# Kernel optimization log

Measured on AMD Instinct MI355X. Metric: run time of the kernel, lower is better.

Reference implementation:

```python
import jax, jax.numpy as jnp
import numpy as np

HIDDEN = 256
B, SQ, SKV = 8, 2048, 2048
SCALE = float(np.sqrt(HIDDEN / 2.0))  # module uses sqrt(hidden_dim/2)


def setup_inputs() -> dict:
    key = jax.random.key(0)
    ks = jax.random.split(key, 9)
    s = 1.0 / np.sqrt(HIDDEN)
    return {
        "query": jax.random.normal(ks[0], (B, SQ, HIDDEN), jnp.float32),
        "key": jax.random.normal(ks[1], (B, SKV, HIDDEN), jnp.float32),
        "value": jax.random.normal(ks[2], (B, SKV, HIDDEN), jnp.float32),
        "Wq": jax.random.uniform(ks[3], (HIDDEN, HIDDEN), jnp.float32, -s, s),
        "bq": jax.random.uniform(ks[4], (HIDDEN,), jnp.float32, -s, s),
        "Wk": jax.random.uniform(ks[5], (HIDDEN, HIDDEN), jnp.float32, -s, s),
        "bk": jax.random.uniform(ks[6], (HIDDEN,), jnp.float32, -s, s),
        "Wv": jax.random.uniform(ks[7], (HIDDEN, HIDDEN), jnp.float32, -s, s),
        "bv": jax.random.uniform(ks[8], (HIDDEN,), jnp.float32, -s, s),
    }


def reference(query, key, value, Wq, bq, Wk, bk, Wv, bv):
    # Linear projections (torch Linear: x @ W.T + b)
    Q = jnp.einsum('bsd,ed->bse', query, Wq) + bq  # [B,SQ,H]
    K = jnp.einsum('bsd,ed->bse', key, Wk) + bk    # [B,SKV,H]
    V = jnp.einsum('bsd,ed->bse', value, Wv) + bv  # [B,SKV,H]
    scores = jnp.einsum('bqd,bkd->bqk', Q, K) / SCALE  # [B,SQ,SKV]
    weights = jax.nn.softmax(scores, axis=-1)
    return jnp.einsum('bqk,bkd->bqd', weights, V)  # [B,SQ,H]
```

## Files before the change

kernel.cpp:

```cpp
#include <hip/hip_runtime.h>

#define HID 256
#define NB 8
#define SQL 2048
#define SKV 2048
#define SPLIT 4
#define KPB (SKV / SPLIT)
#define KVB 32
#define NT (KPB / KVB)
#define NROW (NB * SQL)

typedef __attribute__((ext_vector_type(8))) short bf16x8;
typedef __attribute__((ext_vector_type(4))) float f32x4;

static __device__ __forceinline__ unsigned short f2bf(float x) {
  union { float f; unsigned int u; } v; v.f = x;
  unsigned int r = v.u + 0x7FFFu + ((v.u >> 16) & 1u);
  return (unsigned short)(r >> 16);
}

__global__ void wconv_kernel(const float* __restrict__ Wq, const float* __restrict__ Wk,
                             const float* __restrict__ Wv, unsigned short* __restrict__ out) {
  int i = blockIdx.x * blockDim.x + threadIdx.x;
  if (i >= 3 * HID * HID) return;
  const float* src = (i < HID * HID) ? Wq : (i < 2 * HID * HID ? Wk : Wv);
  out[i] = f2bf(src[i & (HID * HID - 1)]);
}

__global__ __launch_bounds__(512, 4) void proj_kernel(
    const float* __restrict__ query, const float* __restrict__ key, const float* __restrict__ value,
    const unsigned short* __restrict__ Wb,
    const float* __restrict__ bq, const float* __restrict__ bk, const float* __restrict__ bv,
    unsigned short* __restrict__ Qb, unsigned short* __restrict__ Kb, unsigned short* __restrict__ Vtb) {
  __shared__ __align__(16) char wl[65536];
  int tid = threadIdx.x;
  int wave = tid >> 6, lane = tid & 63, lr = lane & 15, lg = lane >> 4;
  int blk = blockIdx.x;
  int mat = blk >> 8;
  int rem = blk & 255;
  int b = rem >> 5;
  int rt = (rem >> 1) & 15;
  int et = rem & 1;

  const float* X = (mat == 0) ? query : (mat == 1 ? key : value);
  const float* bias = (mat == 0) ? bq : (mat == 1 ? bk : bv);
  const char* Wsrc = (const char*)(Wb + mat * HID * HID + et * 128 * HID);

#pragma unroll
  for (int i = 0; i < 8; i++) {
    int c = i * 512 + tid;
    int e = c >> 5;
    int glo = e * 512 + (((c & 31) ^ (e & 7)) << 4);
    __builtin_amdgcn_global_load_lds(
        (const __attribute__((address_space(1))) unsigned int*)(Wsrc + glo),
        (__attribute__((address_space(3))) unsigned int*)(wl + c * 16), 16, 0, 0);
  }

  int row_a = rt * 128 + wave * 16 + lr;
  const float* xrow = X + ((size_t)(b * SQL + row_a)) * HID;
  bf16x8 af[8];
#pragma unroll
  for (int s = 0; s < 8; s++) {
    const float4* p = (const float4*)(xrow + s * 32 + lg * 8);
    float4 x0 = p[0], x1 = p[1];
    bf16x8 a;
    a[0] = (short)f2bf(x0.x); a[1] = (short)f2bf(x0.y); a[2] = (short)f2bf(x0.z); a[3] = (short)f2bf(x0.w);
    a[4] = (short)f2bf(x1.x); a[5] = (short)f2bf(x1.y); a[6] = (short)f2bf(x1.z); a[7] = (short)f2bf(x1.w);
    af[s] = a;
  }
  __syncthreads();

  int row_c = rt * 128 + wave * 16 + lg * 4;
#pragma unroll
  for (int eo = 0; eo < 8; eo++) {
    f32x4 acc = (f32x4){0.f, 0.f, 0.f, 0.f};
    int eL = eo * 16 + lr;
#pragma unroll
    for (int sl = 0; sl < 8; sl++) {
      bf16x8 bfr = *(const bf16x8*)(wl + eL * 512 + (((sl * 4 + lg) ^ (eL & 7)) << 4));
      acc = __builtin_amdgcn_mfma_f32_16x16x32_bf16(af[sl], bfr, acc, 0, 0, 0);
    }
    int e = et * 128 + eo * 16 + lr;
    float bv_ = bias[e];
    if (mat < 2) {
      unsigned short* dst = (mat == 0 ? Qb : Kb) + (size_t)(b * SQL) * HID;
#pragma unroll
      for (int i = 0; i < 4; i++)
        dst[(size_t)(row_c + i) * HID + e] = f2bf(acc[i] + bv_);
    } else {
      ushort4 v;
      v.x = f2bf(acc[0] + bv_); v.y = f2bf(acc[1] + bv_);
      v.z = f2bf(acc[2] + bv_); v.w = f2bf(acc[3] + bv_);
      *(ushort4*)(Vtb + ((size_t)(b * HID + e)) * SKV + row_c) = v;
    }
  }
}

__global__ __launch_bounds__(256, 2) void attn_kernel(
    const unsigned short* __restrict__ Qb, const unsigned short* __restrict__ Kb,
    const unsigned short* __restrict__ Vtb, unsigned short* __restrict__ Op,
    float* __restrict__ Ml) {
  extern __shared__ char smem[];
  int tid = threadIdx.x;
  int wave = tid >> 6, lane = tid & 63, l15 = lane & 15, g = lane >> 4;
  int L = (blockIdx.x & 7) * 64 + (blockIdx.x >> 3);
  int b = L >> 6, sp = (L >> 4) & 3, qt = L & 15;
  int q0 = qt * 128 + wave * 32;

  const char* Kc0 = (const char*)(Kb + ((size_t)b * SKV + (size_t)sp * KPB) * HID);
  const char* Vc0 = (const char*)(Vtb + (size_t)b * HID * SKV + (size_t)sp * KPB);

  int offK[4], offV[4];
#pragma unroll
  for (int i = 0; i < 4; i++) {
    int idx = i * 256 + tid;
    int r = idx >> 5, cs = idx & 31;
    int sig = 8 * ((r & 15) >> 2) + (r & 3) + 4 * (r >> 4);
    offK[i] = sig * 512 + ((cs ^ r) << 4);
    int rv = idx >> 3, pp = idx & 7;
    int p = pp ^ (rv & 7);
    int d = 2 * rv + (p >> 2), c = p & 3;
    offV[i] = d * (SKV * 2) + c * 16;
  }

  auto stage = [&](int t, char* kb, char* vb) {
    const char* Ks = Kc0 + t * (KVB * HID * 2);
    const char* Vs = Vc0 + t * (KVB * 2);
#pragma unroll
    for (int i = 0; i < 4; i++)
      __builtin_amdgcn_global_load_lds(
          (const __attribute__((address_space(1))) unsigned int*)(Ks + offK[i]),
          (__attribute__((address_space(3))) unsigned int*)(kb + (i * 256 + tid) * 16),
          16, 0, 0);
#pragma unroll
    for (int i = 0; i < 4; i++)
      __builtin_amdgcn_global_load_lds(
          (const __attribute__((address_space(1))) unsigned int*)(Vs + offV[i]),
          (__attribute__((address_space(3))) unsigned int*)(vb + (i * 256 + tid) * 16),
          16, 0, 0);
  };

  bf16x8 qfa[8], qfb[8];
  {
    const unsigned short* qa = Qb + ((size_t)(b * SQL + q0 + l15)) * HID + g * 8;
    const unsigned short* qb2 = qa + 16 * HID;
#pragma unroll
    for (int s = 0; s < 8; s++) {
      qfa[s] = *(const bf16x8*)(qa + s * 32);
      qfb[s] = *(const bf16x8*)(qb2 + s * 32);
    }
  }

  f32x4 acc0[16], acc1[16];
#pragma unroll
  for (int dt = 0; dt < 16; dt++) {
    acc0[dt] = (f32x4){0.f, 0.f, 0.f, 0.f};
    acc1[dt] = (f32x4){0.f, 0.f, 0.f, 0.f};
  }
  float m0 = -1e30f, l0 = 0.f, m1 = -1e30f, l1 = 0.f;
  const float kC = 1.44269504088896341f / 11.3137084989847604f;

  auto step = [&](const char* kb, const char* vb) {
    f32x4 p0a = (f32x4){0.f,0.f,0.f,0.f}, p1a = (f32x4){0.f,0.f,0.f,0.f};
    f32x4 p0b = (f32x4){0.f,0.f,0.f,0.f}, p1b = (f32x4){0.f,0.f,0.f,0.f};
#pragma unroll
    for (int s = 0; s < 8; s++) {
      int c0 = s * 4 + g;
      bf16x8 kf0 = *(const bf16x8*)(kb + l15 * 512 + ((c0 ^ l15) << 4));
      bf16x8 kf1 = *(const bf16x8*)(kb + (16 + l15) * 512 + (((c0 ^ l15) ^ 16) << 4));
      p0a = __builtin_amdgcn_mfma_f32_16x16x32_bf16(kf0, qfa[s], p0a, 0, 0, 0);
      p1a = __builtin_amdgcn_mfma_f32_16x16x32_bf16(kf1, qfa[s], p1a, 0, 0, 0);
      p0b = __builtin_amdgcn_mfma_f32_16x16x32_bf16(kf0, qfb[s], p0b, 0, 0, 0);
      p1b = __builtin_amdgcn_mfma_f32_16x16x32_bf16(kf1, qfb[s], p1b, 0, 0, 0);
    }

    float ta = fmaxf(fmaxf(fmaxf(p0a[0], p0a[1]), fmaxf(p0a[2], p0a[3])),
                     fmaxf(fmaxf(p1a[0], p1a[1]), fmaxf(p1a[2], p1a[3])));
    float tb = fmaxf(fmaxf(fmaxf(p0b[0], p0b[1]), fmaxf(p0b[2], p0b[3])),
                     fmaxf(fmaxf(p1b[0], p1b[1]), fmaxf(p1b[2], p1b[3])));
    ta = fmaxf(ta, __shfl_xor(ta, 16, 64)); tb = fmaxf(tb, __shfl_xor(tb, 16, 64));
    ta = fmaxf(ta, __shfl_xor(ta, 32, 64)); tb = fmaxf(tb, __shfl_xor(tb, 32, 64));
    float msa = ta * kC, msb = tb * kC;
    if (!__all(msa <= m0 + 8.0f)) {
      float mn = fmaxf(m0, msa);
      float al = exp2f(m0 - mn);
      l0 *= al; m0 = mn;
#pragma unroll
      for (int dt = 0; dt < 16; dt++)
#pragma unroll
        for (int i = 0; i < 4; i++) acc0[dt][i] *= al;
    }
    if (!__all(msb <= m1 + 8.0f)) {
      float mn = fmaxf(m1, msb);
      float al = exp2f(m1 - mn);
      l1 *= al; m1 = mn;
#pragma unroll
      for (int dt = 0; dt < 16; dt++)
#pragma unroll
        for (int i = 0; i < 4; i++) acc1[dt][i] *= al;
    }
#pragma unroll
    for (int i = 0; i < 4; i++) {
      p0a[i] = exp2f(fmaf(p0a[i], kC, -m0)); p1a[i] = exp2f(fmaf(p1a[i], kC, -m0));
      p0b[i] = exp2f(fmaf(p0b[i], kC, -m1)); p1b[i] = exp2f(fmaf(p1b[i], kC, -m1));
    }
    float sa = (p0a[0] + p0a[1]) + (p0a[2] + p0a[3]) + (p1a[0] + p1a[1]) + (p1a[2] + p1a[3]);
    float sb = (p0b[0] + p0b[1]) + (p0b[2] + p0b[3]) + (p1b[0] + p1b[1]) + (p1b[2] + p1b[3]);
    sa += __shfl_xor(sa, 16, 64); sb += __shfl_xor(sb, 16, 64);
    sa += __shfl_xor(sa, 32, 64); sb += __shfl_xor(sb, 32, 64);
    l0 += sa; l1 += sb;

    unsigned wa0, wa1, wa2, wa3, wb0, wb1, wb2, wb3;
    asm("v_cvt_pk_bf16_f32 %0, %1, %2" : "=v"(wa0) : "v"(p0a[0]), "v"(p0a[1]));
    asm("v_cvt_pk_bf16_f32 %0, %1, %2" : "=v"(wa1) : "v"(p0a[2]), "v"(p0a[3]));
    asm("v_cvt_pk_bf16_f32 %0, %1, %2" : "=v"(wa2) : "v"(p1a[0]), "v"(p1a[1]));
    asm("v_cvt_pk_bf16_f32 %0, %1, %2" : "=v"(wa3) : "v"(p1a[2]), "v"(p1a[3]));
    asm("v_cvt_pk_bf16_f32 %0, %1, %2" : "=v"(wb0) : "v"(p0b[0]), "v"(p0b[1]));
    asm("v_cvt_pk_bf16_f32 %0, %1, %2" : "=v"(wb1) : "v"(p0b[2]), "v"(p0b[3]));
    asm("v_cvt_pk_bf16_f32 %0, %1, %2" : "=v"(wb2) : "v"(p1b[0]), "v"(p1b[1]));
    asm("v_cvt_pk_bf16_f32 %0, %1, %2" : "=v"(wb3) : "v"(p1b[2]), "v"(p1b[3]));
    union { unsigned u[4]; bf16x8 v; } pa, pb;
    pa.u[0] = wa0; pa.u[1] = wa1; pa.u[2] = wa2; pa.u[3] = wa3;
    pb.u[0] = wb0; pb.u[1] = wb1; pb.u[2] = wb2; pb.u[3] = wb3;

    int vsw = ((((l15 & 1) << 2) | g) ^ ((l15 >> 1) & 7)) << 4;
    int vbase = (l15 >> 1) * 128 + vsw;
#pragma unroll
    for (int dt = 0; dt < 16; dt++) {
      bf16x8 vf = *(const bf16x8*)(vb + dt * 1024 + vbase);
      acc0[dt] = __builtin_amdgcn_mfma_f32_16x16x32_bf16(vf, pa.v, acc0[dt], 0, 0, 0);
      acc1[dt] = __builtin_amdgcn_mfma_f32_16x16x32_bf16(vf, pb.v, acc1[dt], 0, 0, 0);
    }
  };

  stage(0, smem, smem + 32768);
  __syncthreads();
  for (int t = 0; t < NT; t++) {
    char* kb = smem + (t & 1) * 16384;
    char* vb = smem + 32768 + (t & 1) * 16384;
    if (t + 1 < NT)
      stage(t + 1, smem + ((t + 1) & 1) * 16384, smem + 32768 + ((t + 1) & 1) * 16384);
    step(kb, vb);
    __syncthreads();
  }

  size_t rowA = (size_t)b * SQL + q0 + l15;
  size_t rowB = rowA + 16;
  if (g == 0) {
    float2 mlA; mlA.x = m0; mlA.y = l0;
    float2 mlB; mlB.x = m1; mlB.y = l1;
    *(float2*)(Ml + ((size_t)sp * NROW + rowA) * 2) = mlA;
    *(float2*)(Ml + ((size_t)sp * NROW + rowB) * 2) = mlB;
  }
  float li0 = 1.0f / l0, li1 = 1.0f / l1;
  unsigned short* oA = Op + ((size_t)sp * NROW + rowA) * HID;
  unsigned short* oB = Op + ((size_t)sp * NROW + rowB) * HID;
#pragma unroll
  for (int dt = 0; dt < 16; dt++) {
    ushort4 v0, v1;
    union { _Float16 hf; unsigned short u; } c;
    c.hf = (_Float16)(acc0[dt][0] * li0); v0.x = c.u;
    c.hf = (_Float16)(acc0[dt][1] * li0); v0.y = c.u;
    c.hf = (_Float16)(acc0[dt][2] * li0); v0.z = c.u;
    c.hf = (_Float16)(acc0[dt][3] * li0); v0.w = c.u;
    c.hf = (_Float16)(acc1[dt][0] * li1); v1.x = c.u;
    c.hf = (_Float16)(acc1[dt][1] * li1); v1.y = c.u;
    c.hf = (_Float16)(acc1[dt][2] * li1); v1.z = c.u;
    c.hf = (_Float16)(acc1[dt][3] * li1); v1.w = c.u;
    *(ushort4*)(oA + dt * 16 + g * 4) = v0;
    *(ushort4*)(oB + dt * 16 + g * 4) = v1;
  }
}

__global__ __launch_bounds__(256) void comb_kernel(const unsigned short* __restrict__ Op,
                                                   const float* __restrict__ Ml,
                                                   float* __restrict__ out) {
  int idx = blockIdx.x * 256 + threadIdx.x;
  int row = idx >> 6;
  int d0 = (idx & 63) << 2;
  float mv[SPLIT], lv[SPLIT];
#pragma unroll
  for (int s = 0; s < SPLIT; s++) {
    float2 ml = *(const float2*)(Ml + ((size_t)s * NROW + row) * 2);
    mv[s] = ml.x; lv[s] = ml.y;
  }
  float M = mv[0];
#pragma unroll
  for (int s = 1; s < SPLIT; s++) M = fmaxf(M, mv[s]);
  float W = 0.f, w[SPLIT];
#pragma unroll
  for (int s = 0; s < SPLIT; s++) { w[s] = lv[s] * exp2f(mv[s] - M); W += w[s]; }
  float wi = 1.0f / W;
  float o0 = 0.f, o1 = 0.f, o2 = 0.f, o3 = 0.f;
#pragma unroll
  for (int s = 0; s < SPLIT; s++) {
    ushort4 u = *(const ushort4*)(Op + ((size_t)s * NROW + row) * HID + d0);
    union { unsigned short us; _Float16 hf; } c0, c1, c2, c3;
    c0.us = u.x; c1.us = u.y; c2.us = u.z; c3.us = u.w;
    o0 += w[s] * (float)c0.hf; o1 += w[s] * (float)c1.hf;
    o2 += w[s] * (float)c2.hf; o3 += w[s] * (float)c3.hf;
  }
  float4 res; res.x = o0 * wi; res.y = o1 * wi; res.z = o2 * wi; res.w = o3 * wi;
  *(float4*)(out + (size_t)row * HID + d0) = res;
}

extern "C" void kernel_launch(void* const* d_in, const int* in_sizes, int n_in,
                              void* d_out, int out_size, void* d_ws, size_t ws_size,
                              hipStream_t stream) {
  const float* query = (const float*)d_in[0];
  const float* key   = (const float*)d_in[1];
  const float* value = (const float*)d_in[2];
  const float* Wq = (const float*)d_in[3];
  const float* bq = (const float*)d_in[4];
  const float* Wk = (const float*)d_in[5];
  const float* bk = (const float*)d_in[6];
  const float* Wv = (const float*)d_in[7];
  const float* bv = (const float*)d_in[8];

  char* ws = (char*)d_ws;
  unsigned short* Wb  = (unsigned short*)ws;
  unsigned short* Qb  = (unsigned short*)(ws + 393216);
  unsigned short* Kb  = Qb + (size_t)NB * SQL * HID;
  unsigned short* Vtb = Kb + (size_t)NB * SKV * HID;
  unsigned short* Op  = Vtb + (size_t)NB * HID * SKV;
  float* Ml = (float*)(Op + (size_t)SPLIT * NROW * HID);

  hipLaunchKernelGGL(wconv_kernel, dim3(768), dim3(256), 0, stream, Wq, Wk, Wv, Wb);
  hipLaunchKernelGGL(proj_kernel, dim3(768), dim3(512), 0, stream,
                     query, key, value, Wb, bq, bk, bv, Qb, Kb, Vtb);
  hipLaunchKernelGGL(attn_kernel, dim3(512), dim3(256), 65536, stream, Qb, Kb, Vtb, Op, Ml);
  hipLaunchKernelGGL(comb_kernel, dim3(4096), dim3(256), 0, stream, Op, Ml, (float*)d_out);
}
```

Measured before the change: 103.8 us.

## Store K and V in MFMA fragment order so attention loads are contiguous

The projection kernel now writes K and V directly in the per-lane MFMA fragment layout that the attention kernel consumes, instead of row-major K and transposed V. Attention staging then becomes a plain contiguous 16 KB copy per tile, and the LDS reads become lane-linear without XOR swizzle arithmetic. This removes the strided, scattered global gathers and the address math in the inner loop. The cost is that the projection epilogue now does scattered 2-byte stores for K and V, which may hurt write coalescing there. LDS bank conflicts also change now that the swizzle is gone.

New measurement: 92.24 us. 11.2% less time.

```diff
diff --git a/kernel.cpp b/kernel.cpp
--- a/kernel.cpp
+++ b/kernel.cpp
@@ -31,7 +31,7 @@
     const float* __restrict__ query, const float* __restrict__ key, const float* __restrict__ value,
     const unsigned short* __restrict__ Wb,
     const float* __restrict__ bq, const float* __restrict__ bk, const float* __restrict__ bv,
-    unsigned short* __restrict__ Qb, unsigned short* __restrict__ Kb, unsigned short* __restrict__ Vtb) {
+    unsigned short* __restrict__ Qb, unsigned short* __restrict__ KFo, unsigned short* __restrict__ VFo) {
   __shared__ __align__(16) char wl[65536];
   int tid = threadIdx.x;
   int wave = tid >> 6, lane = tid & 63, lr = lane & 15, lg = lane >> 4;
@@ -82,23 +82,38 @@
     }
     int e = et * 128 + eo * 16 + lr;
     float bv_ = bias[e];
-    if (mat < 2) {
-      unsigned short* dst = (mat == 0 ? Qb : Kb) + (size_t)(b * SQL) * HID;
+    if (mat == 0) {
+      unsigned short* dst = Qb + (size_t)(b * SQL) * HID;
 #pragma unroll
       for (int i = 0; i < 4; i++)
         dst[(size_t)(row_c + i) * HID + e] = f2bf(acc[i] + bv_);
+    } else if (mat == 1) {
+      int s = e >> 5, gg = (e >> 3) & 3, j = e & 7;
+#pragma unroll
+      for (int i = 0; i < 4; i++) {
+        int row = row_c + i;
+        int k5 = row & 31;
+        int half = (k5 >> 2) & 1;
+        int lidx = (((k5 >> 3) << 2) | (k5 & 3)) + 16 * gg;
+        size_t frag = (size_t)(b * 1024 + (row >> 5) * 16 + half * 8 + s);
+        KFo[frag * 512 + lidx * 8 + j] = f2bf(acc[i] + bv_);
+      }
     } else {
-      ushort4 v;
-      v.x = f2bf(acc[0] + bv_); v.y = f2bf(acc[1] + bv_);
-      v.z = f2bf(acc[2] + bv_); v.w = f2bf(acc[3] + bv_);
-      *(ushort4*)(Vtb + ((size_t)(b * HID + e)) * SKV + row_c) = v;
+      int dt = e >> 4, l15 = e & 15;
+#pragma unroll
+      for (int i = 0; i < 4; i++) {
+        int row = row_c + i;
+        int gg = (row >> 3) & 3, j = row & 7;
+        size_t frag = (size_t)(b * 1024 + (row >> 5) * 16 + dt);
+        VFo[frag * 512 + (l15 + 16 * gg) * 8 + j] = f2bf(acc[i] + bv_);
+      }
     }
   }
 }
 
 __global__ __launch_bounds__(256, 2) void attn_kernel(
-    const unsigned short* __restrict__ Qb, const unsigned short* __restrict__ Kb,
-    const unsigned short* __restrict__ Vtb, unsigned short* __restrict__ Op,
+    const unsigned short* __restrict__ Qb, const char* __restrict__ KF,
+    const char* __restrict__ VF, unsigned short* __restrict__ Op,
     float* __restrict__ Ml) {
   extern __shared__ char smem[];
   int tid = threadIdx.x;
@@ -107,36 +122,23 @@
   int b = L >> 6, sp = (L >> 4) & 3, qt = L & 15;
   int q0 = qt * 128 + wave * 32;
 
-  const char* Kc0 = (const char*)(Kb + ((size_t)b * SKV + (size_t)sp * KPB) * HID);
-  const char* Vc0 = (const char*)(Vtb + (size_t)b * HID * SKV + (size_t)sp * KPB);
-
-  int offK[4], offV[4];
-#pragma unroll
-  for (int i = 0; i < 4; i++) {
-    int idx = i * 256 + tid;
-    int r = idx >> 5, cs = idx & 31;
-    int sig = 8 * ((r & 15) >> 2) + (r & 3) + 4 * (r >> 4);
-    offK[i] = sig * 512 + ((cs ^ r) << 4);
-    int rv = idx >> 3, pp = idx & 7;
-    int p = pp ^ (rv & 7);
-    int d = 2 * rv + (p >> 2), c = p & 3;
-    offV[i] = d * (SKV * 2) + c * 16;
-  }
+  const char* Ks0 = KF + ((size_t)(b * 64 + sp * 16)) * 16384;
+  const char* Vs0 = VF + ((size_t)(b * 64 + sp * 16)) * 16384;
 
   auto stage = [&](int t, char* kb, char* vb) {
-    const char* Ks = Kc0 + t * (KVB * HID * 2);
-    const char* Vs = Vc0 + t * (KVB * 2);
+    const char* Ks = Ks0 + (size_t)t * 16384;
+    const char* Vs = Vs0 + (size_t)t * 16384;
 #pragma unroll
     for (int i = 0; i < 4; i++)
       __builtin_amdgcn_global_load_lds(
-          (const __attribute__((address_space(1))) unsigned int*)(Ks + offK[i]),
-          (__attribute__((address_space(3))) unsigned int*)(kb + (i * 256 + tid) * 16),
+          (const __attribute__((address_space(1))) unsigned int*)(Ks + i * 4096 + tid * 16),
+          (__attribute__((address_space(3))) unsigned int*)(kb + i * 4096 + tid * 16),
           16, 0, 0);
 #pragma unroll
     for (int i = 0; i < 4; i++)
       __builtin_amdgcn_global_load_lds(
-          (const __attribute__((address_space(1))) unsigned int*)(Vs + offV[i]),
-          (__attribute__((address_space(3))) unsigned int*)(vb + (i * 256 + tid) * 16),
+          (const __attribute__((address_space(1))) unsigned int*)(Vs + i * 4096 + tid * 16),
+          (__attribute__((address_space(3))) unsigned int*)(vb + i * 4096 + tid * 16),
           16, 0, 0);
   };
 
@@ -161,13 +163,14 @@
   const float kC = 1.44269504088896341f / 11.3137084989847604f;
 
   auto step = [&](const char* kb, const char* vb) {
+    const char* kbl = kb + lane * 16;
+    const char* vbl = vb + lane * 16;
     f32x4 p0a = (f32x4){0.f,0.f,0.f,0.f}, p1a = (f32x4){0.f,0.f,0.f,0.f};
     f32x4 p0b = (f32x4){0.f,0.f,0.f,0.f}, p1b = (f32x4){0.f,0.f,0.f,0.f};
 #pragma unroll
     for (int s = 0; s < 8; s++) {
-      int c0 = s * 4 + g;
-      bf16x8 kf0 = *(const bf16x8*)(kb + l15 * 512 + ((c0 ^ l15) << 4));
-      bf16x8 kf1 = *(const bf16x8*)(kb + (16 + l15) * 512 + (((c0 ^ l15) ^ 16) << 4));
+      bf16x8 kf0 = *(const bf16x8*)(kbl + s * 1024);
+      bf16x8 kf1 = *(const bf16x8*)(kbl + (8 + s) * 1024);
       p0a = __builtin_amdgcn_mfma_f32_16x16x32_bf16(kf0, qfa[s], p0a, 0, 0, 0);
       p1a = __builtin_amdgcn_mfma_f32_16x16x32_bf16(kf1, qfa[s], p1a, 0, 0, 0);
       p0b = __builtin_amdgcn_mfma_f32_16x16x32_bf16(kf0, qfb[s], p0b, 0, 0, 0);
@@ -223,11 +226,9 @@
     pa.u[0] = wa0; pa.u[1] = wa1; pa.u[2] = wa2; pa.u[3] = wa3;
     pb.u[0] = wb0; pb.u[1] = wb1; pb.u[2] = wb2; pb.u[3] = wb3;
 
-    int vsw = ((((l15 & 1) << 2) | g) ^ ((l15 >> 1) & 7)) << 4;
-    int vbase = (l15 >> 1) * 128 + vsw;
 #pragma unroll
     for (int dt = 0; dt < 16; dt++) {
-      bf16x8 vf = *(const bf16x8*)(vb + dt * 1024 + vbase);
+      bf16x8 vf = *(const bf16x8*)(vbl + dt * 1024);
       acc0[dt] = __builtin_amdgcn_mfma_f32_16x16x32_bf16(vf, pa.v, acc0[dt], 0, 0, 0);
       acc1[dt] = __builtin_amdgcn_mfma_f32_16x16x32_bf16(vf, pb.v, acc1[dt], 0, 0, 0);
     }
@@ -320,14 +321,15 @@
   char* ws = (char*)d_ws;
   unsigned short* Wb  = (unsigned short*)ws;
   unsigned short* Qb  = (unsigned short*)(ws + 393216);
-  unsigned short* Kb  = Qb + (size_t)NB * SQL * HID;
-  unsigned short* Vtb = Kb + (size_t)NB * SKV * HID;
-  unsigned short* Op  = Vtb + (size_t)NB * HID * SKV;
+  unsigned short* KF  = Qb + (size_t)NB * SQL * HID;
+  unsigned short* VF  = KF + (size_t)NB * SKV * HID;
+  unsigned short* Op  = VF + (size_t)NB * HID * SKV;
   float* Ml = (float*)(Op + (size_t)SPLIT * NROW * HID);
 
   hipLaunchKernelGGL(wconv_kernel, dim3(768), dim3(256), 0, stream, Wq, Wk, Wv, Wb);
   hipLaunchKernelGGL(proj_kernel, dim3(768), dim3(512), 0, stream,
-                     query, key, value, Wb, bq, bk, bv, Qb, Kb, Vtb);
-  hipLaunchKernelGGL(attn_kernel, dim3(512), dim3(256), 65536, stream, Qb, Kb, Vtb, Op, Ml);
+                     query, key, value, Wb, bq, bk, bv, Qb, KF, VF);
+  hipLaunchKernelGGL(attn_kernel, dim3(512), dim3(256), 65536, stream,
+                     Qb, (const char*)KF, (const char*)VF, Op, Ml);
   hipLaunchKernelGGL(comb_kernel, dim3(4096), dim3(256), 0, stream, Op, Ml, (float*)d_out);
 }
```
